# Kernel optimization log

Hardware: AMD Instinct MI355X
Metric: run time of the kernel (lower is better)

## Reference

```python
import jax, jax.numpy as jnp
import numpy as np

IN_DIM, OUT_DIM, H, K, N = 2048, 2048, 8192, 256, 4096


def _w_eff(codebook, idx, frozen_mask, int8_mask, int8_vals, w_float, alpha):
    looked = codebook[idx]
    merged = jnp.where(int8_mask, alpha * int8_vals, w_float)
    return jnp.where(frozen_mask, looked, merged)


def _c19(x, c_raw, rho_raw):
    c = jnp.maximum(c_raw, 0.1)
    rho = jnp.maximum(rho_raw, 0.0)
    L = 6.0 * c
    scaled = x / c
    n = jnp.floor(scaled)
    t = scaled - n
    h = t * (1.0 - t)
    # torch: n.long() % 2 == 0 -> +1 else -1 (python-style modulo, same as jnp.mod)
    sgn = jnp.where(jnp.mod(n.astype(jnp.int32), 2) == 0, 1.0, -1.0)
    interior = c * (sgn * h + rho * h * h)
    return jnp.where(x >= L, x - L, jnp.where(x <= -L, x + L, interior))


def setup_inputs() -> dict:
    key = jax.random.key(0)
    ks = jax.random.split(key, 16)
    x = jax.random.normal(ks[0], (N, IN_DIM), dtype=jnp.float32)
    codebook_W1 = jax.random.normal(ks[1], (K,), dtype=jnp.float32) * 0.02
    codebook_W2 = jax.random.normal(ks[2], (K,), dtype=jnp.float32) * 0.02
    W1_idx = jax.random.randint(ks[3], (IN_DIM, H), 0, K)
    W2_idx = jax.random.randint(ks[4], (H, OUT_DIM), 0, K)
    W1_frozen_mask = jax.random.bernoulli(ks[5], 0.5, (IN_DIM, H))
    W2_frozen_mask = jax.random.bernoulli(ks[6], 0.5, (H, OUT_DIM))
    W1_int8_mask = jax.random.bernoulli(ks[7], 0.25, (IN_DIM, H))
    W2_int8_mask = jax.random.bernoulli(ks[8], 0.25, (H, OUT_DIM))
    # quantized levels (stored as float32 buffers in the torch module)
    W1_int8 = jnp.round(jnp.clip(jax.random.normal(ks[9], (IN_DIM, H)) * 40.0, -127, 127))
    W2_int8 = jnp.round(jnp.clip(jax.random.normal(ks[10], (H, OUT_DIM)) * 40.0, -127, 127))
    W1_float = jax.random.normal(ks[11], (IN_DIM, H), dtype=jnp.float32) * 0.02
    W2_float = jax.random.normal(ks[12], (H, OUT_DIM), dtype=jnp.float32) * 0.02
    # alpha = max(|free float cells|)/127 as in __init__ (mask out frozen cells)
    a1 = jnp.maximum(jnp.abs(jnp.where(W1_frozen_mask, 0.0, W1_float)).max() / 127.0, 1e-6)
    a2 = jnp.maximum(jnp.abs(jnp.where(W2_frozen_mask, 0.0, W2_float)).max() / 127.0, 1e-6)
    b1 = jax.random.normal(ks[13], (H,), dtype=jnp.float32) * 0.01
    b2 = jax.random.normal(ks[14], (OUT_DIM,), dtype=jnp.float32) * 0.01
    db1 = jax.random.normal(ks[15], (H,), dtype=jnp.float32) * 0.01
    db2 = jax.random.normal(jax.random.fold_in(key, 99), (IN_DIM,), dtype=jnp.float32) * 0.01
    c_raw = jnp.full((H,), 1.0, dtype=jnp.float32)
    rho_raw = jnp.full((H,), 8.0, dtype=jnp.float32)
    return {
        "x": x, "codebook_W1": codebook_W1, "codebook_W2": codebook_W2,
        "W1_idx": W1_idx, "W2_idx": W2_idx,
        "W1_frozen_mask": W1_frozen_mask, "W2_frozen_mask": W2_frozen_mask,
        "W1_int8_mask": W1_int8_mask, "W2_int8_mask": W2_int8_mask,
        "W1_int8": W1_int8, "W2_int8": W2_int8,
        "W1_float": W1_float, "W2_float": W2_float,
        "alpha_free_W1": a1, "alpha_free_W2": a2,
        "b1": b1, "b2": b2, "db1": db1, "db2": db2,
        "c_raw": c_raw, "rho_raw": rho_raw,
    }


def reference(x, codebook_W1, codebook_W2, W1_idx, W2_idx,
              W1_frozen_mask, W2_frozen_mask, W1_int8_mask, W2_int8_mask,
              W1_int8, W2_int8, W1_float, W2_float,
              alpha_free_W1, alpha_free_W2, b1, b2, db1, db2, c_raw, rho_raw):
    W1 = _w_eff(codebook_W1, W1_idx, W1_frozen_mask, W1_int8_mask, W1_int8, W1_float, alpha_free_W1)
    W2 = _w_eff(codebook_W2, W2_idx, W2_frozen_mask, W2_int8_mask, W2_int8, W2_float, alpha_free_W2)
    # encode
    z = _c19(x @ W1 + b1, c_raw, rho_raw) @ W2 + b2          # [N, out_dim]
    # decode
    dec = (z @ W2.T + db1) @ W1.T + db2                      # [N, in_dim]
    return (dec, z)
```

## Files before the change

### kernel.cpp

```cpp
#include <hip/hip_runtime.h>

#define AS1 __attribute__((address_space(1)))
#define AS3 __attribute__((address_space(3)))

typedef __attribute__((ext_vector_type(8))) short short8;
typedef __attribute__((ext_vector_type(8))) float float8;
typedef __attribute__((ext_vector_type(8))) int int8v;
typedef __attribute__((ext_vector_type(4))) float f32x4;
typedef __attribute__((ext_vector_type(4))) unsigned short u16x4;

__device__ __forceinline__ unsigned short f2bf(float f) {
  union { float f; unsigned u; } v; v.f = f;
  return (unsigned short)((v.u + 0x7fffu + ((v.u >> 16) & 1u)) >> 16);
}

__device__ __forceinline__ void gload_lds16(const void* g, void* l) {
  __builtin_amdgcn_global_load_lds((const AS1 unsigned*)g, (AS3 unsigned*)l, 16, 0, 0);
}

#define MEMFENCE asm volatile("" ::: "memory")
#define BARRIER() do { MEMFENCE; __builtin_amdgcn_s_barrier(); MEMFENCE; } while (0)

__global__ void detect_fmt(const unsigned char* __restrict__ m, int* __restrict__ flag) {
  __shared__ int found;
  if (threadIdx.x == 0) found = 0;
  __syncthreads();
  for (int i = threadIdx.x; i < 4096; i += 256)
    if ((i & 3) != 0 && m[i] != 0) found = 1;
  __syncthreads();
  if (threadIdx.x == 0) flag[0] = found;
}

__global__ __launch_bounds__(256) void build_w2(
    const float* __restrict__ cb, const int* __restrict__ idx,
    const unsigned char* __restrict__ fz8, const unsigned char* __restrict__ im8,
    const float* __restrict__ i8v, const float* __restrict__ wf,
    const float* __restrict__ alpha_p, const int* __restrict__ flag_p,
    unsigned short* __restrict__ w_nat, unsigned short* __restrict__ w_t,
    int R, int C) {
  __shared__ float cbs[256];
  __shared__ float tile[64][65];
  const int t = threadIdx.x;
  cbs[t] = cb[t];
  const int rBase = blockIdx.y * 64, cBase = blockIdx.x * 64;
  const float alpha = alpha_p[0];
  const int isU8 = flag_p[0];
  __syncthreads();
#pragma unroll
  for (int p = 0; p < 2; ++p) {
    const int rl = p * 32 + (t >> 3);
    const int cl = (t & 7) * 8;
    const size_t off = (size_t)(rBase + rl) * C + cBase + cl;
    float8 wv = *(const float8*)(wf + off);
    float8 qv = *(const float8*)(i8v + off);
    int8v iv = *(const int8v*)(idx + off);
    unsigned fzm[8], imm[8];
    if (isU8) {
      unsigned long long fm = *(const unsigned long long*)(fz8 + off);
      unsigned long long im = *(const unsigned long long*)(im8 + off);
#pragma unroll
      for (int k = 0; k < 8; ++k) { fzm[k] = (fm >> (8 * k)) & 255ull; imm[k] = (im >> (8 * k)) & 255ull; }
    } else {
      int8v fv = *(const int8v*)((const int*)fz8 + off);
      int8v mv = *(const int8v*)((const int*)im8 + off);
#pragma unroll
      for (int k = 0; k < 8; ++k) { fzm[k] = fv[k]; imm[k] = mv[k]; }
    }
    short8 o;
#pragma unroll
    for (int k = 0; k < 8; ++k) {
      float r = fzm[k] ? cbs[iv[k] & 255] : (imm[k] ? alpha * qv[k] : wv[k]);
      o[k] = (short)f2bf(r);
      tile[rl][cl + k] = r;
    }
    *(short8*)(w_nat + off) = o;
  }
  __syncthreads();
#pragma unroll
  for (int p = 0; p < 2; ++p) {
    const int cl = p * 32 + (t >> 3);
    const int r0 = (t & 7) * 8;
    short8 o;
#pragma unroll
    for (int j = 0; j < 8; ++j) o[j] = (short)f2bf(tile[r0 + j][cl]);
    *(short8*)(w_t + (size_t)(cBase + cl) * R + rBase + r0) = o;
  }
}

__global__ __launch_bounds__(256) void cvt_bf16(const float* __restrict__ in,
                                                unsigned short* __restrict__ out, int n4) {
  int i = blockIdx.x * 256 + threadIdx.x;
  if (i < n4) {
    float4 v = ((const float4*)in)[i];
    u16x4 r;
    r.x = f2bf(v.x); r.y = f2bf(v.y); r.z = f2bf(v.z); r.w = f2bf(v.w);
    ((u16x4*)out)[i] = r;
  }
}

template <int WITHB16>
__global__ __launch_bounds__(256) void combine(
    const float* __restrict__ p0, const float* __restrict__ p1,
    const float* __restrict__ bias, float* __restrict__ outF,
    unsigned short* __restrict__ outB, int Nmask, int n4) {
  for (int i = blockIdx.x * 256 + threadIdx.x; i < n4; i += gridDim.x * 256) {
    float4 a = ((const float4*)p0)[i];
    float4 b = ((const float4*)p1)[i];
    float4 bv = *(const float4*)(bias + ((i * 4) & Nmask));
    float4 v;
    v.x = a.x + b.x + bv.x; v.y = a.y + b.y + bv.y;
    v.z = a.z + b.z + bv.z; v.w = a.w + b.w + bv.w;
    ((float4*)outF)[i] = v;
    if constexpr (WITHB16) {
      u16x4 r;
      r.x = f2bf(v.x); r.y = f2bf(v.y); r.z = f2bf(v.z); r.w = f2bf(v.w);
      ((u16x4*)outB)[i] = r;
    }
  }
}

template <int MODE, int SPLIT>
__global__ __launch_bounds__(512, 2) void gemm8(
    const unsigned short* __restrict__ A, const unsigned short* __restrict__ Bt,
    int M, int N, int K,
    const float* __restrict__ bias,
    const float* __restrict__ c_raw, const float* __restrict__ rho_raw,
    unsigned short* __restrict__ outB,
    float* __restrict__ pF0, float* __restrict__ pF1) {
  extern __shared__ unsigned short lds8[];
  const int t = threadIdx.x;
  const int l = t & 63, w = t >> 6;
  const int wm = w >> 2, wn = w & 3;
  const int lr = l & 15, q = l >> 4;

  const int nwg = gridDim.x;
  const int id = (blockIdx.x & 7) * (nwg >> 3) + (blockIdx.x >> 3);
  int tileId, slice, kBase;
  if constexpr (SPLIT == 2) { tileId = id >> 1; slice = id & 1; kBase = slice * (K >> 1); }
  else { tileId = id; slice = 0; kBase = 0; }
  const int nbx = N >> 8;
  const int tileM = (tileId / nbx) * 256, tileN = (tileId % nbx) * 256;
  const int Keff = K / SPLIT;

  f32x4 acc[8][4];
#pragma unroll
  for (int mi = 0; mi < 8; ++mi)
#pragma unroll
    for (int ni = 0; ni < 4; ++ni) acc[mi][ni] = (f32x4){0.f, 0.f, 0.f, 0.f};

  const int srow = l >> 3, sslot = l & 7;
  const unsigned short* aSrc[2];
  const unsigned short* bSrc[2];
  int ldsOff[2];
#pragma unroll
  for (int i = 0; i < 2; ++i) {
    int rl = w * 16 + i * 8 + srow;
    int sl = sslot ^ (rl & 7);
    aSrc[i] = A + (size_t)(tileM + rl) * K + kBase + sl * 8;
    bSrc[i] = Bt + (size_t)(tileN + rl) * K + kBase + sl * 8;
    ldsOff[i] = (w * 2 + i) * 512;
  }
  const size_t dK = (size_t)128 * K;

#define STAGE_A0(buf, kt) { gload_lds16(aSrc[0] + (kt), lds8 + (buf)*32768 + 0*8192 + ldsOff[0]); \
                            gload_lds16(aSrc[1] + (kt), lds8 + (buf)*32768 + 0*8192 + ldsOff[1]); }
#define STAGE_A1(buf, kt) { gload_lds16(aSrc[0] + dK + (kt), lds8 + (buf)*32768 + 1*8192 + ldsOff[0]); \
                            gload_lds16(aSrc[1] + dK + (kt), lds8 + (buf)*32768 + 1*8192 + ldsOff[1]); }
#define STAGE_B0(buf, kt) { gload_lds16(bSrc[0] + (kt), lds8 + (buf)*32768 + 2*8192 + ldsOff[0]); \
                            gload_lds16(bSrc[1] + (kt), lds8 + (buf)*32768 + 2*8192 + ldsOff[1]); }
#define STAGE_B1(buf, kt) { gload_lds16(bSrc[0] + dK + (kt), lds8 + (buf)*32768 + 3*8192 + ldsOff[0]); \
                            gload_lds16(bSrc[1] + dK + (kt), lds8 + (buf)*32768 + 3*8192 + ldsOff[1]); }

  const int sw = (lr & 7) << 4;
  const int k0 = (q * 16) ^ sw;
  const int k1 = (64 + q * 16) ^ sw;
  const char* ldsc = (const char*)lds8;
  const int bRowBase = (wn & 1) * 64;

  const int nt = Keff >> 6;
  STAGE_A0(0, 0); STAGE_A1(0, 0); STAGE_B0(0, 0); STAGE_B1(0, 0);
  {
    int kt1 = (nt > 1) ? 64 : 0;
    STAGE_B0(1, kt1); STAGE_B1(1, kt1);
  }
  asm volatile("s_waitcnt vmcnt(4)" ::: "memory");
  BARRIER();

  short8 af[4][2], bf[4][2];
  for (int tt = 0; tt < nt; ++tt) {
    const int cur = tt & 1, nx = cur ^ 1;
    const int ktA = (tt + 1 < nt ? tt + 1 : 0) << 6;
    const int ktB = (tt + 2 < nt ? tt + 2 : 0) << 6;
    const int aB = cur * 65536 + wm * 16384;
    const int bB = cur * 65536 + 32768 + (wn >> 1) * 16384;

#pragma unroll
    for (int mi = 0; mi < 4; ++mi) {
      af[mi][0] = *(const short8*)(ldsc + aB + (mi * 16 + lr) * 128 + k0);
      af[mi][1] = *(const short8*)(ldsc + aB + (mi * 16 + lr) * 128 + k1);
    }
#pragma unroll
    for (int ni = 0; ni < 2; ++ni) {
      bf[ni][0] = *(const short8*)(ldsc + bB + (bRowBase + ni * 16 + lr) * 128 + k0);
      bf[ni][1] = *(const short8*)(ldsc + bB + (bRowBase + ni * 16 + lr) * 128 + k1);
    }
    STAGE_A0(nx, ktA);
    BARRIER();
    asm volatile("s_waitcnt lgkmcnt(0)" ::: "memory");
    __builtin_amdgcn_s_setprio(1);
#pragma unroll
    for (int mi = 0; mi < 4; ++mi)
#pragma unroll
      for (int ni = 0; ni < 2; ++ni) {
        acc[mi][ni] = __builtin_amdgcn_mfma_f32_16x16x32_bf16(af[mi][0], bf[ni][0], acc[mi][ni], 0, 0, 0);
        acc[mi][ni] = __builtin_amdgcn_mfma_f32_16x16x32_bf16(af[mi][1], bf[ni][1], acc[mi][ni], 0, 0, 0);
      }
    __builtin_amdgcn_s_setprio(0);
    BARRIER();

#pragma unroll
    for (int ni = 2; ni < 4; ++ni) {
      bf[ni][0] = *(const short8*)(ldsc + bB + (bRowBase + ni * 16 + lr) * 128 + k0);
      bf[ni][1] = *(const short8*)(ldsc + bB + (bRowBase + ni * 16 + lr) * 128 + k1);
    }
    STAGE_A1(nx, ktA);
    BARRIER();
    asm volatile("s_waitcnt lgkmcnt(0)" ::: "memory");
    __builtin_amdgcn_s_setprio(1);
#pragma unroll
    for (int mi = 0; mi < 4; ++mi)
#pragma unroll
      for (int ni = 2; ni < 4; ++ni) {
        acc[mi][ni] = __builtin_amdgcn_mfma_f32_16x16x32_bf16(af[mi][0], bf[ni][0], acc[mi][ni], 0, 0, 0);
        acc[mi][ni] = __builtin_amdgcn_mfma_f32_16x16x32_bf16(af[mi][1], bf[ni][1], acc[mi][ni], 0, 0, 0);
      }
    __builtin_amdgcn_s_setprio(0);
    BARRIER();

#pragma unroll
    for (int mi = 0; mi < 4; ++mi) {
      af[mi][0] = *(const short8*)(ldsc + aB + ((mi + 4) * 16 + lr) * 128 + k0);
      af[mi][1] = *(const short8*)(ldsc + aB + ((mi + 4) * 16 + lr) * 128 + k1);
    }
    STAGE_B0(cur, ktB);
    BARRIER();
    asm volatile("s_waitcnt lgkmcnt(0)" ::: "memory");
    __builtin_amdgcn_s_setprio(1);
#pragma unroll
    for (int mi = 0; mi < 4; ++mi)
#pragma unroll
      for (int ni = 2; ni < 4; ++ni) {
        acc[mi + 4][ni] = __builtin_amdgcn_mfma_f32_16x16x32_bf16(af[mi][0], bf[ni][0], acc[mi + 4][ni], 0, 0, 0);
        acc[mi + 4][ni] = __builtin_amdgcn_mfma_f32_16x16x32_bf16(af[mi][1], bf[ni][1], acc[mi + 4][ni], 0, 0, 0);
      }
    __builtin_amdgcn_s_setprio(0);
    BARRIER();

    STAGE_B1(cur, ktB);
    BARRIER();
    __builtin_amdgcn_s_setprio(1);
#pragma unroll
    for (int mi = 0; mi < 4; ++mi)
#pragma unroll
      for (int ni = 0; ni < 2; ++ni) {
        acc[mi + 4][ni] = __builtin_amdgcn_mfma_f32_16x16x32_bf16(af[mi][0], bf[ni][0], acc[mi + 4][ni], 0, 0, 0);
        acc[mi + 4][ni] = __builtin_amdgcn_mfma_f32_16x16x32_bf16(af[mi][1], bf[ni][1], acc[mi + 4][ni], 0, 0, 0);
      }
    __builtin_amdgcn_s_setprio(0);
    asm volatile("s_waitcnt vmcnt(4)" ::: "memory");
    BARRIER();
  }
#undef STAGE_A0
#undef STAGE_A1
#undef STAGE_B0
#undef STAGE_B1

  float* pOut = nullptr;
  if constexpr (MODE == 4) pOut = slice ? pF1 : pF0;
#pragma unroll
  for (int ni = 0; ni < 4; ++ni) {
    const int col = tileN + wn * 64 + ni * 16 + lr;
    float bv = 0.f, cc = 0.f, rr = 0.f, L = 0.f;
    if constexpr (MODE == 0 || MODE == 2) bv = bias[col];
    if constexpr (MODE == 0) {
      cc = fmaxf(c_raw[col], 0.1f);
      rr = fmaxf(rho_raw[col], 0.0f);
      L = 6.0f * cc;
    }
#pragma unroll
    for (int mi = 0; mi < 8; ++mi) {
      const int row0 = tileM + wm * 128 + mi * 16 + q * 4;
#pragma unroll
      for (int j = 0; j < 4; ++j) {
        float v = acc[mi][ni][j] + bv;
        size_t off = (size_t)(row0 + j) * N + col;
        if constexpr (MODE == 0) {
          float scaled = v / cc;
          float fn = floorf(scaled);
          float ttf = scaled - fn;
          float h = ttf * (1.0f - ttf);
          int ip = (int)fn;
          float sgn = (ip & 1) ? -1.0f : 1.0f;
          float interior = cc * (sgn * h + rr * h * h);
          float res = (v >= L) ? (v - L) : ((v <= -L) ? (v + L) : interior);
          outB[off] = f2bf(res);
        } else if constexpr (MODE == 2) {
          outB[off] = f2bf(v);
        } else {
          pOut[off] = v;
        }
      }
    }
  }
}

extern "C" void kernel_launch(void* const* d_in, const int* in_sizes, int n_in,
                              void* d_out, int out_size, void* d_ws, size_t ws_size,
                              hipStream_t stream) {
  (void)in_sizes; (void)n_in; (void)out_size; (void)ws_size;
  const float* x = (const float*)d_in[0];
  const float* cb1 = (const float*)d_in[1];
  const float* cb2 = (const float*)d_in[2];
  const int* idx1 = (const int*)d_in[3];
  const int* idx2 = (const int*)d_in[4];
  const unsigned char* fz1 = (const unsigned char*)d_in[5];
  const unsigned char* fz2 = (const unsigned char*)d_in[6];
  const unsigned char* im1 = (const unsigned char*)d_in[7];
  const unsigned char* im2 = (const unsigned char*)d_in[8];
  const float* i8v1 = (const float*)d_in[9];
  const float* i8v2 = (const float*)d_in[10];
  const float* wf1 = (const float*)d_in[11];
  const float* wf2 = (const float*)d_in[12];
  const float* a1 = (const float*)d_in[13];
  const float* a2 = (const float*)d_in[14];
  const float* b1 = (const float*)d_in[15];
  const float* b2 = (const float*)d_in[16];
  const float* db1 = (const float*)d_in[17];
  const float* db2 = (const float*)d_in[18];
  const float* c_raw = (const float*)d_in[19];
  const float* rho_raw = (const float*)d_in[20];

  char* ws = (char*)d_ws;
  const size_t WSZ = 33554432;
  unsigned short* W1T = (unsigned short*)(ws + 0 * WSZ);
  unsigned short* W1N = (unsigned short*)(ws + 1 * WSZ);
  unsigned short* W2T = (unsigned short*)(ws + 2 * WSZ);
  unsigned short* W2N = (unsigned short*)(ws + 3 * WSZ);
  unsigned short* XB = (unsigned short*)(ws + 4 * WSZ);
  unsigned short* H = (unsigned short*)(ws + 4 * WSZ + 16777216);
  unsigned short* ZB = (unsigned short*)(ws + 4 * WSZ + 16777216 + 67108864);
  int* flag = (int*)(ws + 4 * WSZ + 16777216 + 67108864 + 16777216);
  float* dec = (float*)d_out;
  float* zf = (float*)d_out + 8388608;

  (void)hipFuncSetAttribute((const void*)gemm8<0, 1>, hipFuncAttributeMaxDynamicSharedMemorySize, 131072);
  (void)hipFuncSetAttribute((const void*)gemm8<2, 1>, hipFuncAttributeMaxDynamicSharedMemorySize, 131072);
  (void)hipFuncSetAttribute((const void*)gemm8<4, 2>, hipFuncAttributeMaxDynamicSharedMemorySize, 131072);

  detect_fmt<<<1, 256, 0, stream>>>(fz1, flag);
  build_w2<<<dim3(8192 / 64, 2048 / 64), 256, 0, stream>>>(cb1, idx1, fz1, im1, i8v1, wf1, a1, flag, W1N, W1T, 2048, 8192);
  build_w2<<<dim3(2048 / 64, 8192 / 64), 256, 0, stream>>>(cb2, idx2, fz2, im2, i8v2, wf2, a2, flag, W2N, W2T, 8192, 2048);
  cvt_bf16<<<8192, 256, 0, stream>>>(x, XB, 2097152);

  gemm8<0, 1><<<512, 512, 131072, stream>>>(XB, W1T, 4096, 8192, 2048, b1, c_raw, rho_raw, H, nullptr, nullptr);
  gemm8<4, 2><<<256, 512, 131072, stream>>>(H, W2T, 4096, 2048, 8192, nullptr, nullptr, nullptr, nullptr, zf, (float*)W1T);
  combine<1><<<2048, 256, 0, stream>>>(zf, (float*)W1T, b2, zf, ZB, 2047, 2097152);
  gemm8<2, 1><<<512, 512, 131072, stream>>>(ZB, W2N, 4096, 8192, 2048, db1, nullptr, nullptr, H, nullptr, nullptr);
  gemm8<4, 2><<<256, 512, 131072, stream>>>(H, W1N, 4096, 2048, 8192, nullptr, nullptr, nullptr, nullptr, dec, (float*)W2T);
  combine<0><<<2048, 256, 0, stream>>>(dec, (float*)W2T, db2, dec, nullptr, 2047, 2097152);
}
```

Baseline: 1.183 ms.

## Stage bf16 epilogue through LDS for 16-byte stores and remap tiles per XCD

```diff
diff --git a/kernel.cpp b/kernel.cpp
--- a/kernel.cpp
+++ b/kernel.cpp
@@ -8,6 +8,7 @@
 typedef __attribute__((ext_vector_type(8))) int int8v;
 typedef __attribute__((ext_vector_type(4))) float f32x4;
 typedef __attribute__((ext_vector_type(4))) unsigned short u16x4;
+typedef __attribute__((ext_vector_type(8))) unsigned short u16x8;
 
 __device__ __forceinline__ unsigned short f2bf(float f) {
   union { float f; unsigned u; } v; v.f = f;
@@ -133,13 +134,20 @@
   const int wm = w >> 2, wn = w & 3;
   const int lr = l & 15, q = l >> 4;
 
-  const int nwg = gridDim.x;
-  const int id = (blockIdx.x & 7) * (nwg >> 3) + (blockIdx.x >> 3);
-  int tileId, slice, kBase;
-  if constexpr (SPLIT == 2) { tileId = id >> 1; slice = id & 1; kBase = slice * (K >> 1); }
-  else { tileId = id; slice = 0; kBase = 0; }
-  const int nbx = N >> 8;
-  const int tileM = (tileId / nbx) * 256, tileN = (tileId % nbx) * 256;
+  const int xcd = blockIdx.x & 7;
+  const int local = blockIdx.x >> 3;
+  int tileM, tileN, slice, kBase;
+  if constexpr (SPLIT == 2) {
+    slice = local & 1;
+    const int tl = local >> 1;
+    tileM = (((xcd >> 1) << 2) + (tl >> 2)) << 8;
+    tileN = (((xcd & 1) << 2) + (tl & 3)) << 8;
+    kBase = slice * (K >> 1);
+  } else {
+    slice = 0; kBase = 0;
+    tileM = (((xcd >> 2) << 3) + (local >> 3)) << 8;
+    tileN = (((xcd & 3) << 3) + (local & 7)) << 8;
+  }
   const int Keff = K / SPLIT;
 
   f32x4 acc[8][4];
@@ -275,40 +283,66 @@
 #undef STAGE_B0
 #undef STAGE_B1
 
-  float* pOut = nullptr;
-  if constexpr (MODE == 4) pOut = slice ? pF1 : pF0;
-#pragma unroll
-  for (int ni = 0; ni < 4; ++ni) {
-    const int col = tileN + wn * 64 + ni * 16 + lr;
-    float bv = 0.f, cc = 0.f, rr = 0.f, L = 0.f;
-    if constexpr (MODE == 0 || MODE == 2) bv = bias[col];
-    if constexpr (MODE == 0) {
-      cc = fmaxf(c_raw[col], 0.1f);
-      rr = fmaxf(rho_raw[col], 0.0f);
-      L = 6.0f * cc;
-    }
+  if constexpr (MODE == 0 || MODE == 2) {
+    float bv4[4], cc4[4], rr4[4], L4[4];
+#pragma unroll
+    for (int ni = 0; ni < 4; ++ni) {
+      const int col = tileN + wn * 64 + ni * 16 + lr;
+      bv4[ni] = bias[col];
+      if constexpr (MODE == 0) {
+        cc4[ni] = fmaxf(c_raw[col], 0.1f);
+        rr4[ni] = fmaxf(rho_raw[col], 0.0f);
+        L4[ni] = 6.0f * cc4[ni];
+      }
+    }
+    asm volatile("s_waitcnt vmcnt(0)" ::: "memory");
+    BARRIER();
+    unsigned short* sc = lds8 + w * 1152;
 #pragma unroll
     for (int mi = 0; mi < 8; ++mi) {
-      const int row0 = tileM + wm * 128 + mi * 16 + q * 4;
-#pragma unroll
-      for (int j = 0; j < 4; ++j) {
-        float v = acc[mi][ni][j] + bv;
-        size_t off = (size_t)(row0 + j) * N + col;
-        if constexpr (MODE == 0) {
-          float scaled = v / cc;
-          float fn = floorf(scaled);
-          float ttf = scaled - fn;
-          float h = ttf * (1.0f - ttf);
-          int ip = (int)fn;
-          float sgn = (ip & 1) ? -1.0f : 1.0f;
-          float interior = cc * (sgn * h + rr * h * h);
-          float res = (v >= L) ? (v - L) : ((v <= -L) ? (v + L) : interior);
-          outB[off] = f2bf(res);
-        } else if constexpr (MODE == 2) {
-          outB[off] = f2bf(v);
-        } else {
-          pOut[off] = v;
+#pragma unroll
+      for (int ni = 0; ni < 4; ++ni)
+#pragma unroll
+        for (int j = 0; j < 4; ++j) {
+          float v = acc[mi][ni][j] + bv4[ni];
+          float res;
+          if constexpr (MODE == 0) {
+            float scaled = v / cc4[ni];
+            float fn = floorf(scaled);
+            float ttf = scaled - fn;
+            float h = ttf * (1.0f - ttf);
+            int ip = (int)fn;
+            float sgn = (ip & 1) ? -1.0f : 1.0f;
+            float interior = cc4[ni] * (sgn * h + rr4[ni] * h * h);
+            res = (v >= L4[ni]) ? (v - L4[ni]) : ((v <= -L4[ni]) ? (v + L4[ni]) : interior);
+          } else {
+            res = v;
+          }
+          sc[(q * 4 + j) * 72 + ni * 16 + lr] = f2bf(res);
         }
+      asm volatile("s_waitcnt lgkmcnt(0)" ::: "memory");
+#pragma unroll
+      for (int sgi = 0; sgi < 2; ++sgi) {
+        const int s = sgi * 64 + l;
+        const int r = s >> 3, cs = (s & 7) * 8;
+        u16x8 vv = *(const u16x8*)(sc + r * 72 + cs);
+        const int row = tileM + wm * 128 + mi * 16 + r;
+        const int col = tileN + wn * 64 + cs;
+        *(u16x8*)(outB + (size_t)row * N + col) = vv;
+      }
+      asm volatile("s_waitcnt lgkmcnt(0)" ::: "memory");
+    }
+  } else {
+    float* pOut = slice ? pF1 : pF0;
+#pragma unroll
+    for (int ni = 0; ni < 4; ++ni) {
+      const int col = tileN + wn * 64 + ni * 16 + lr;
+#pragma unroll
+      for (int mi = 0; mi < 8; ++mi) {
+        const int row0 = tileM + wm * 128 + mi * 16 + q * 4;
+#pragma unroll
+        for (int j = 0; j < 4; ++j)
+          pOut[(size_t)(row0 + j) * N + col] = acc[mi][ni][j];
       }
     }
   }
```

Result: faster. 1.144 ms (-3.3%).
